# Kernel tuning notes

Measured on AMD Instinct MI355X. Metric: run time of the kernel, lower is better.

## Reference

```python
import jax, jax.numpy as jnp
import numpy as np

CONF_THRESH = 0.3
NMS_THRESH = 0.5
TOP_K = 64
VAR = (0.1, 0.2)  # standard SSD decode variances


def setup_inputs() -> dict:
    key = jax.random.key(0)
    k1, k2, k3 = jax.random.split(key, 3)
    B, A, C = 16, 16384, 81
    loc = jax.random.normal(k1, (B, A, 4), jnp.float32)
    conf = jax.random.normal(k2, (B, A, C), jnp.float32)
    anchors = jax.random.uniform(k3, (A, 4), jnp.float32)  # cxcywh in [0,1]
    return {"loc": loc, "conf": conf, "anchors": anchors}


def _decode(loc, anchors):
    # SSD-style decode: loc [A,4] offsets, anchors [A,4] cxcywh -> corners [A,4]
    cxcy = anchors[:, :2] + loc[:, :2] * VAR[0] * anchors[:, 2:]
    wh = anchors[:, 2:] * jnp.exp(loc[:, 2:] * VAR[1])
    tl = cxcy - wh * 0.5
    return jnp.concatenate([tl, tl + wh], axis=1)


def _iou(box, boxes):
    # box [4], boxes [A,4] in corner format
    tl = jnp.maximum(box[:2], boxes[:, :2])
    br = jnp.minimum(box[2:], boxes[:, 2:])
    wh = jnp.clip(br - tl, 0.0)
    inter = wh[:, 0] * wh[:, 1]
    a1 = (box[2] - box[0]) * (box[3] - box[1])
    a2 = (boxes[:, 2] - boxes[:, 0]) * (boxes[:, 3] - boxes[:, 1])
    return inter / (a1 + a2 - inter)


def _nms(boxes, scores):
    # greedy NMS for one (batch, class) lane; boxes [A,4], scores [A]
    s0 = jnp.where(scores > CONF_THRESH, scores, -1.0)

    def step(s, _):
        i = jnp.argmax(s)
        sc = s[i]
        box = boxes[i]
        keep = sc > 0.0  # -1 means masked/suppressed; valid scores > conf_thresh > 0
        supp = jnp.where(_iou(box, boxes) > NMS_THRESH, -1.0, s).at[i].set(-1.0)
        s_next = jnp.where(keep, supp, s)
        row = jnp.where(keep, jnp.concatenate([sc[None], box]),
                        jnp.zeros((5,), s.dtype))
        return s_next, row

    _, rows = jax.lax.scan(step, s0, None, length=TOP_K)
    return rows  # [TOP_K, 5] = (score, x1, y1, x2, y2), zero-padded


def reference(loc, conf, anchors):
    conf = jax.nn.sigmoid(conf)                      # [B,A,C]
    boxes = jax.vmap(_decode, in_axes=(0, None))(loc, anchors)  # [B,A,4]
    scores = jnp.swapaxes(conf, 1, 2)                # [B,C,A]
    per_class = jax.vmap(_nms, in_axes=(None, 0))    # over classes
    out = jax.vmap(per_class)(boxes, scores)         # [B,C,TOP_K,5]
    return out
```

## Files before the change

### kernel.cpp

```cpp
#include <hip/hip_runtime.h>
#include <math.h>

constexpr int B_N  = 16;
constexpr int A_N  = 16384;
constexpr int C_N  = 81;
constexpr int TOPK = 64;
constexpr int DNT  = 256;
constexpr int NBINS = 232;
constexpr int CAP   = 512;
constexpr unsigned BIN_BASE = 0x3E99u;

constexpr int TA   = 128;
constexpr int TPAD = 85;
constexpr int TNT  = 256;
constexpr int TILE_ELEMS = TA * C_N;
constexpr int TILE_F4    = (TA / 4) * C_N;

constexpr int HNT = 256;

__global__ __launch_bounds__(DNT) void decode_kernel(const float4* __restrict__ loc,
                                                     const float4* __restrict__ anch,
                                                     float4* __restrict__ boxes) {
    int i = blockIdx.x * DNT + threadIdx.x;
    int a = i & (A_N - 1);
    float4 l  = loc[i];
    float4 an = anch[a];
    float cx = an.x + (l.x * 0.1f) * an.z;
    float cy = an.y + (l.y * 0.1f) * an.w;
    float w  = an.z * expf(l.z * 0.2f);
    float h  = an.w * expf(l.w * 0.2f);
    float x1 = cx - w * 0.5f;
    float y1 = cy - h * 0.5f;
    boxes[i] = make_float4(x1, y1, x1 + w, y1 + h);
}

__global__ __launch_bounds__(TNT) void sigT_kernel(const float* __restrict__ conf,
                                                   float* __restrict__ scoresT) {
    __shared__ float tile[TA][TPAD];

    const int a0 = blockIdx.x * TA;
    const int b  = blockIdx.y;
    const int t  = threadIdx.x;

    const float* src = conf + ((size_t)b * A_N + a0) * C_N;
#pragma unroll
    for (int i = 0; i < (TILE_ELEMS + TNT - 1) / TNT; ++i) {
        int idx = i * TNT + t;
        if (idx < TILE_ELEMS) {
            float x  = src[idx];
            int   al = idx / C_N;
            int   cc = idx - al * C_N;
            tile[al][cc] = 1.0f / (1.0f + expf(-x));
        }
    }
    __syncthreads();
    float* dst = scoresT + (size_t)b * C_N * A_N + a0;
#pragma unroll
    for (int i = 0; i < (TILE_F4 + TNT - 1) / TNT; ++i) {
        int idx4 = i * TNT + t;
        if (idx4 < TILE_F4) {
            int cc  = idx4 >> 5;
            int al4 = idx4 & 31;
            float4 v;
            v.x = tile[al4 * 4 + 0][cc];
            v.y = tile[al4 * 4 + 1][cc];
            v.z = tile[al4 * 4 + 2][cc];
            v.w = tile[al4 * 4 + 3][cc];
            ((float4*)(dst + (size_t)cc * A_N))[al4] = v;
        }
    }
}

__global__ __launch_bounds__(HNT) void hist_kernel(const float* __restrict__ scoresT,
                                                   int* __restrict__ ghist) {
    __shared__ int hist[NBINS];
    const int bc = blockIdx.x;
    const int t  = threadIdx.x;
    for (int i = t; i < NBINS; i += HNT) hist[i] = 0;
    __syncthreads();
    const float4* sptr = (const float4*)(scoresT + (size_t)bc * A_N);
    for (int i = 0; i < A_N / 4 / HNT; ++i) {
        float4 s4 = sptr[t + HNT * i];
        float s[4] = {s4.x, s4.y, s4.z, s4.w};
#pragma unroll
        for (int q = 0; q < 4; ++q) {
            if (s[q] > 0.3f) {
                unsigned u = __float_as_uint(s[q]);
                int bin = (int)(u >> 16) - (int)BIN_BASE;
                bin = bin < 0 ? 0 : (bin > NBINS - 1 ? NBINS - 1 : bin);
                atomicAdd(&hist[bin], 1);
            }
        }
    }
    __syncthreads();
    int* g = ghist + (size_t)bc * NBINS;
    for (int i = t; i < NBINS; i += HNT) g[i] = hist[i];
}

template <bool TRANSPOSED>
__global__ __launch_bounds__(64, 4) void nms_kernel(const float* __restrict__ conf,
                                                    const float* __restrict__ scoresT,
                                                    const int* __restrict__ ghist,
                                                    const float4* __restrict__ boxes,
                                                    float* __restrict__ out) {
    __shared__ int hist[NBINS];
    __shared__ unsigned long long cand[CAP];
    __shared__ float4 cbox[CAP];
    __shared__ int s_cnt;

    const int c    = blockIdx.x;
    const int b    = blockIdx.y;
    const int lane = threadIdx.x;

    const float4* bptr = boxes + (size_t)b * A_N;
    const float4* sptr = (const float4*)(scoresT + ((size_t)b * C_N + c) * A_N);
    const float*  cptr = conf + (size_t)b * A_N * C_N + c;
    float* optr = out + ((size_t)(b * C_N + c)) * TOPK * 5;

    if (TRANSPOSED) {
        const int* g = ghist + (size_t)(b * C_N + c) * NBINS;
        for (int i = lane; i < NBINS; i += 64) hist[i] = g[i];
    } else {
        for (int i = lane; i < NBINS; i += 64) hist[i] = 0;
        __syncthreads();
        for (int i = 0; i < A_N / 256; ++i) {
            int a0 = 4 * (lane + 64 * i);
#pragma unroll
            for (int q = 0; q < 4; ++q) {
                float x = cptr[(size_t)(a0 + q) * C_N];
                float s = 1.0f / (1.0f + expf(-x));
                if (s > 0.3f) {
                    unsigned u = __float_as_uint(s);
                    int bin = (int)(u >> 16) - (int)BIN_BASE;
                    bin = bin < 0 ? 0 : (bin > NBINS - 1 ? NBINS - 1 : bin);
                    atomicAdd(&hist[bin], 1);
                }
            }
        }
    }
    __syncthreads();

    float rx1 = 0.f, ry1 = 0.f, rx2 = 0.f, ry2 = 0.f, rar = 0.f;
    int acc = 0, kout = 0;

    int bin_hi = NBINS;
    for (;;) {
        int lo = bin_hi, tot = 0;
        while (lo > 0) {
            int cnt = hist[lo - 1];
            if (tot + cnt > CAP) {
                if (tot == 0) { lo--; }
                break;
            }
            tot += cnt; lo--;
        }
        const int bin_lo = lo;
        if (bin_lo == bin_hi) break;
        if (lane == 0) s_cnt = 0;
        __syncthreads();

        for (int i = 0; i < A_N / 256; ++i) {
            float s[4];
            if (TRANSPOSED) {
                float4 s4 = sptr[lane + 64 * i];
                s[0] = s4.x; s[1] = s4.y; s[2] = s4.z; s[3] = s4.w;
            } else {
                int a0 = 4 * (lane + 64 * i);
#pragma unroll
                for (int q = 0; q < 4; ++q) {
                    float x = cptr[(size_t)(a0 + q) * C_N];
                    s[q] = 1.0f / (1.0f + expf(-x));
                }
            }
#pragma unroll
            for (int q = 0; q < 4; ++q) {
                if (s[q] > 0.3f) {
                    unsigned u = __float_as_uint(s[q]);
                    int bin = (int)(u >> 16) - (int)BIN_BASE;
                    bin = bin < 0 ? 0 : (bin > NBINS - 1 ? NBINS - 1 : bin);
                    if (bin >= bin_lo && bin < bin_hi) {
                        int slot = atomicAdd(&s_cnt, 1);
                        if (slot < CAP) {
                            unsigned a = (unsigned)(4 * (lane + 64 * i) + q);
                            cand[slot] = ((unsigned long long)u << 32) | (unsigned)(~a);
                        }
                    }
                }
            }
        }
        __syncthreads();
        int C = s_cnt; if (C > CAP) C = CAP;

        if (C > 0) {
            unsigned long long key[8];
#pragma unroll
            for (int r = 0; r < 8; ++r) {
                int sidx = r * 64 + lane;
                key[r] = (sidx < C) ? cand[sidx] : 0ull;
            }
#pragma unroll
            for (int k = 2; k <= CAP; k <<= 1) {
#pragma unroll
                for (int j = k >> 1; j > 0; j >>= 1) {
                    if (j >= 64) {
                        int jr = j >> 6;
#pragma unroll
                        for (int r = 0; r < 8; ++r) {
                            int rp = r ^ jr;
                            if (rp > r) {
                                int e = r * 64 + lane;
                                bool up = ((e & k) == 0);
                                unsigned long long va = key[r], vb = key[rp];
                                bool sw = up ? (va < vb) : (va > vb);
                                if (sw) { key[r] = vb; key[rp] = va; }
                            }
                        }
                    } else {
#pragma unroll
                        for (int r = 0; r < 8; ++r) {
                            int e = r * 64 + lane;
                            bool up    = ((e & k) == 0);
                            bool isLow = ((lane & j) == 0);
                            unsigned long long va = key[r];
                            unsigned long long vb = __shfl_xor(va, j, 64);
                            bool keepMax = (up == isLow);
                            key[r] = keepMax ? (va > vb ? va : vb)
                                             : (va < vb ? va : vb);
                        }
                    }
                }
            }
            __syncthreads();
#pragma unroll
            for (int r = 0; r < 8; ++r) cand[r * 64 + lane] = key[r];
            __syncthreads();

#pragma unroll
            for (int r = 0; r < 8; ++r) {
                int e = r * 64 + lane;
                if (e < C) {
                    int idx = (int)(~(unsigned)cand[e]);
                    cbox[e] = bptr[idx];
                }
            }
            __syncthreads();

            int t = 0;
            unsigned long long k0 = cand[0];
            float4 cb = cbox[0];
            while (t < C) {
                unsigned long long nk = 0ull;
                float4 nb = cb;
                if (t + 1 < C) { nk = cand[t + 1]; nb = cbox[t + 1]; }
                float sc = __uint_as_float((unsigned)(k0 >> 32));
                float ca = (cb.z - cb.x) * (cb.w - cb.y);
                bool over = false;
                if (lane < acc) {
                    float tlx = fmaxf(rx1, cb.x);
                    float tly = fmaxf(ry1, cb.y);
                    float brx = fminf(rx2, cb.z);
                    float bry = fminf(ry2, cb.w);
                    float iw  = fmaxf(brx - tlx, 0.0f);
                    float ih  = fmaxf(bry - tly, 0.0f);
                    float inter = iw * ih;
                    float iou = inter / (rar + ca - inter);
                    over = iou > 0.5f;
                }
                if (!__any(over)) {
                    if (lane == acc) { rx1 = cb.x; ry1 = cb.y; rx2 = cb.z; ry2 = cb.w; rar = ca; }
                    if (lane == 0) {
                        float* o = optr + (size_t)kout * 5;
                        o[0] = sc; o[1] = cb.x; o[2] = cb.y; o[3] = cb.z; o[4] = cb.w;
                    }
                    acc++; kout++;
                    if (acc == TOPK) break;
                }
                ++t; k0 = nk; cb = nb;
            }
        }
        if (acc == TOPK) break;
        bin_hi = bin_lo;
    }

    {
        float* o  = optr + (size_t)kout * 5;
        int   rem = (TOPK - kout) * 5;
        for (int t = lane; t < rem; t += 64) o[t] = 0.0f;
    }
}

extern "C" void kernel_launch(void* const* d_in, const int* in_sizes, int n_in,
                              void* d_out, int out_size, void* d_ws, size_t ws_size,
                              hipStream_t stream) {
    const float* loc     = (const float*)d_in[0];
    const float* conf    = (const float*)d_in[1];
    const float* anchors = (const float*)d_in[2];
    float* out = (float*)d_out;

    const size_t boxes_bytes  = (size_t)B_N * A_N * sizeof(float4);
    const size_t scores_bytes = (size_t)B_N * C_N * A_N * sizeof(float);
    const size_t hist_bytes   = (size_t)B_N * C_N * NBINS * sizeof(int);

    float4* boxes = (float4*)d_ws;

    decode_kernel<<<(B_N * A_N) / DNT, DNT, 0, stream>>>(
        (const float4*)loc, (const float4*)anchors, boxes);

    if (ws_size >= boxes_bytes + scores_bytes + hist_bytes) {
        float* scoresT = (float*)((char*)d_ws + boxes_bytes);
        int*   ghist   = (int*)((char*)d_ws + boxes_bytes + scores_bytes);
        sigT_kernel<<<dim3(A_N / TA, B_N), TNT, 0, stream>>>(conf, scoresT);
        hist_kernel<<<dim3(B_N * C_N), HNT, 0, stream>>>(scoresT, ghist);
        nms_kernel<true><<<dim3(C_N, B_N), 64, 0, stream>>>(conf, scoresT, ghist, boxes, out);
    } else {
        nms_kernel<false><<<dim3(C_N, B_N), 64, 0, stream>>>(conf, nullptr, nullptr, boxes, out);
    }
}
```

Baseline: 254.3 us.

## Move first-round candidate selection into wide histogram kernel

```diff
diff --git a/kernel.cpp b/kernel.cpp
--- a/kernel.cpp
+++ b/kernel.cpp
@@ -16,7 +16,7 @@
 constexpr int TILE_ELEMS = TA * C_N;
 constexpr int TILE_F4    = (TA / 4) * C_N;
 
-constexpr int HNT = 256;
+constexpr int SNT = 256;
 
 __global__ __launch_bounds__(DNT) void decode_kernel(const float4* __restrict__ loc,
                                                      const float4* __restrict__ anch,
@@ -71,16 +71,20 @@
     }
 }
 
-__global__ __launch_bounds__(HNT) void hist_kernel(const float* __restrict__ scoresT,
-                                                   int* __restrict__ ghist) {
+__global__ __launch_bounds__(SNT) void select_kernel(const float* __restrict__ scoresT,
+                                                     int* __restrict__ ghist,
+                                                     unsigned long long* __restrict__ gcand,
+                                                     int2* __restrict__ gmeta) {
     __shared__ int hist[NBINS];
+    __shared__ int s_cnt;
     const int bc = blockIdx.x;
     const int t  = threadIdx.x;
-    for (int i = t; i < NBINS; i += HNT) hist[i] = 0;
-    __syncthreads();
+    for (int i = t; i < NBINS; i += SNT) hist[i] = 0;
+    __syncthreads();
+
     const float4* sptr = (const float4*)(scoresT + (size_t)bc * A_N);
-    for (int i = 0; i < A_N / 4 / HNT; ++i) {
-        float4 s4 = sptr[t + HNT * i];
+    for (int i = 0; i < A_N / 4 / SNT; ++i) {
+        float4 s4 = sptr[t + SNT * i];
         float s[4] = {s4.x, s4.y, s4.z, s4.w};
 #pragma unroll
         for (int q = 0; q < 4; ++q) {
@@ -94,13 +98,141 @@
     }
     __syncthreads();
     int* g = ghist + (size_t)bc * NBINS;
-    for (int i = t; i < NBINS; i += HNT) g[i] = hist[i];
-}
-
-template <bool TRANSPOSED>
+    for (int i = t; i < NBINS; i += SNT) g[i] = hist[i];
+
+    int lo = NBINS, tot = 0;
+    while (lo > 0) {
+        int cnt = hist[lo - 1];
+        if (tot + cnt > CAP) {
+            if (tot == 0) { lo--; }
+            break;
+        }
+        tot += cnt; lo--;
+    }
+    if (t == 0) s_cnt = 0;
+    __syncthreads();
+
+    unsigned long long* cd = gcand + (size_t)bc * CAP;
+    for (int i = 0; i < A_N / 4 / SNT; ++i) {
+        float4 s4 = sptr[t + SNT * i];
+        float s[4] = {s4.x, s4.y, s4.z, s4.w};
+#pragma unroll
+        for (int q = 0; q < 4; ++q) {
+            if (s[q] > 0.3f) {
+                unsigned u = __float_as_uint(s[q]);
+                int bin = (int)(u >> 16) - (int)BIN_BASE;
+                bin = bin < 0 ? 0 : (bin > NBINS - 1 ? NBINS - 1 : bin);
+                if (bin >= lo) {
+                    int slot = atomicAdd(&s_cnt, 1);
+                    if (slot < CAP) {
+                        unsigned a = (unsigned)(4 * (t + SNT * i) + q);
+                        cd[slot] = ((unsigned long long)u << 32) | (unsigned)(~a);
+                    }
+                }
+            }
+        }
+    }
+    __syncthreads();
+    if (t == 0) {
+        int C = s_cnt; if (C > CAP) C = CAP;
+        gmeta[bc] = make_int2(C, lo);
+    }
+}
+
+__device__ __forceinline__ void sort_gather_scan(
+        unsigned long long* cand, float4* cbox, int C, int lane,
+        const float4* __restrict__ bptr, float* __restrict__ optr,
+        float& rx1, float& ry1, float& rx2, float& ry2, float& rar,
+        int& acc, int& kout) {
+    unsigned long long key[8];
+#pragma unroll
+    for (int r = 0; r < 8; ++r) {
+        int sidx = r * 64 + lane;
+        key[r] = (sidx < C) ? cand[sidx] : 0ull;
+    }
+#pragma unroll
+    for (int k = 2; k <= CAP; k <<= 1) {
+#pragma unroll
+        for (int j = k >> 1; j > 0; j >>= 1) {
+            if (j >= 64) {
+                int jr = j >> 6;
+#pragma unroll
+                for (int r = 0; r < 8; ++r) {
+                    int rp = r ^ jr;
+                    if (rp > r) {
+                        int e = r * 64 + lane;
+                        bool up = ((e & k) == 0);
+                        unsigned long long va = key[r], vb = key[rp];
+                        bool sw = up ? (va < vb) : (va > vb);
+                        if (sw) { key[r] = vb; key[rp] = va; }
+                    }
+                }
+            } else {
+#pragma unroll
+                for (int r = 0; r < 8; ++r) {
+                    int e = r * 64 + lane;
+                    bool up    = ((e & k) == 0);
+                    bool isLow = ((lane & j) == 0);
+                    unsigned long long va = key[r];
+                    unsigned long long vb = __shfl_xor(va, j, 64);
+                    bool keepMax = (up == isLow);
+                    key[r] = keepMax ? (va > vb ? va : vb)
+                                     : (va < vb ? va : vb);
+                }
+            }
+        }
+    }
+    __syncthreads();
+#pragma unroll
+    for (int r = 0; r < 8; ++r) cand[r * 64 + lane] = key[r];
+    __syncthreads();
+#pragma unroll
+    for (int r = 0; r < 8; ++r) {
+        int e = r * 64 + lane;
+        if (e < C) cbox[e] = bptr[(int)(~(unsigned)cand[e])];
+    }
+    __syncthreads();
+
+    int t = 0;
+    unsigned long long k0 = cand[0];
+    float4 cb = cbox[0];
+    while (t < C) {
+        unsigned long long nk = 0ull;
+        float4 nb = cb;
+        if (t + 1 < C) { nk = cand[t + 1]; nb = cbox[t + 1]; }
+        float sc = __uint_as_float((unsigned)(k0 >> 32));
+        float ca = (cb.z - cb.x) * (cb.w - cb.y);
+        bool over = false;
+        if (lane < acc) {
+            float tlx = fmaxf(rx1, cb.x);
+            float tly = fmaxf(ry1, cb.y);
+            float brx = fminf(rx2, cb.z);
+            float bry = fminf(ry2, cb.w);
+            float iw  = fmaxf(brx - tlx, 0.0f);
+            float ih  = fmaxf(bry - tly, 0.0f);
+            float inter = iw * ih;
+            float iou = inter / (rar + ca - inter);
+            over = iou > 0.5f;
+        }
+        if (!__any(over)) {
+            if (lane == acc) { rx1 = cb.x; ry1 = cb.y; rx2 = cb.z; ry2 = cb.w; rar = ca; }
+            if (lane == 0) {
+                float* o = optr + (size_t)kout * 5;
+                o[0] = sc; o[1] = cb.x; o[2] = cb.y; o[3] = cb.z; o[4] = cb.w;
+            }
+            acc++; kout++;
+            if (acc == TOPK) break;
+        }
+        ++t; k0 = nk; cb = nb;
+    }
+}
+
+template <bool PRESEL>
 __global__ __launch_bounds__(64, 4) void nms_kernel(const float* __restrict__ conf,
                                                     const float* __restrict__ scoresT,
                                                     const int* __restrict__ ghist,
+                                                    const unsigned long long* __restrict__ gcand,
+                                                    const int2* __restrict__ gmeta,
                                                     const float4* __restrict__ boxes,
                                                     float* __restrict__ out) {
     __shared__ int hist[NBINS];
@@ -110,16 +242,36 @@
 
     const int c    = blockIdx.x;
     const int b    = blockIdx.y;
+    const int bc   = b * C_N + c;
     const int lane = threadIdx.x;
 
     const float4* bptr = boxes + (size_t)b * A_N;
-    const float4* sptr = (const float4*)(scoresT + ((size_t)b * C_N + c) * A_N);
+    const float4* sptr = (const float4*)(scoresT + (size_t)bc * A_N);
     const float*  cptr = conf + (size_t)b * A_N * C_N + c;
-    float* optr = out + ((size_t)(b * C_N + c)) * TOPK * 5;
-
-    if (TRANSPOSED) {
-        const int* g = ghist + (size_t)(b * C_N + c) * NBINS;
-        for (int i = lane; i < NBINS; i += 64) hist[i] = g[i];
+    float* optr = out + (size_t)bc * TOPK * 5;
+
+    float rx1 = 0.f, ry1 = 0.f, rx2 = 0.f, ry2 = 0.f, rar = 0.f;
+    int acc = 0, kout = 0;
+    int bin_hi;
+
+    if (PRESEL) {
+        int2 meta = gmeta[bc];
+        int C = meta.x;
+        bin_hi = meta.y;
+        const unsigned long long* cd = gcand + (size_t)bc * CAP;
+#pragma unroll
+        for (int r = 0; r < 8; ++r) {
+            int e = r * 64 + lane;
+            cand[e] = (e < C) ? cd[e] : 0ull;
+        }
+        __syncthreads();
+        if (C > 0)
+            sort_gather_scan(cand, cbox, C, lane, bptr, optr,
+                             rx1, ry1, rx2, ry2, rar, acc, kout);
+        if (acc < TOPK && bin_hi > 0) {
+            for (int i = lane; i < NBINS; i += 64) hist[i] = ghist[(size_t)bc * NBINS + i];
+            __syncthreads();
+        }
     } else {
         for (int i = lane; i < NBINS; i += 64) hist[i] = 0;
         __syncthreads();
@@ -137,14 +289,11 @@
                 }
             }
         }
-    }
-    __syncthreads();
-
-    float rx1 = 0.f, ry1 = 0.f, rx2 = 0.f, ry2 = 0.f, rar = 0.f;
-    int acc = 0, kout = 0;
-
-    int bin_hi = NBINS;
-    for (;;) {
+        __syncthreads();
+        bin_hi = NBINS;
+    }
+
+    while (acc < TOPK) {
         int lo = bin_hi, tot = 0;
         while (lo > 0) {
             int cnt = hist[lo - 1];
@@ -161,7 +310,7 @@
 
         for (int i = 0; i < A_N / 256; ++i) {
             float s[4];
-            if (TRANSPOSED) {
+            if (PRESEL) {
                 float4 s4 = sptr[lane + 64 * i];
                 s[0] = s4.x; s[1] = s4.y; s[2] = s4.z; s[3] = s4.w;
             } else {
@@ -190,95 +339,9 @@
         }
         __syncthreads();
         int C = s_cnt; if (C > CAP) C = CAP;
-
-        if (C > 0) {
-            unsigned long long key[8];
-#pragma unroll
-            for (int r = 0; r < 8; ++r) {
-                int sidx = r * 64 + lane;
-                key[r] = (sidx < C) ? cand[sidx] : 0ull;
-            }
-#pragma unroll
-            for (int k = 2; k <= CAP; k <<= 1) {
-#pragma unroll
-                for (int j = k >> 1; j > 0; j >>= 1) {
-                    if (j >= 64) {
-                        int jr = j >> 6;
-#pragma unroll
-                        for (int r = 0; r < 8; ++r) {
-                            int rp = r ^ jr;
-                            if (rp > r) {
-                                int e = r * 64 + lane;
-                                bool up = ((e & k) == 0);
-                                unsigned long long va = key[r], vb = key[rp];
-                                bool sw = up ? (va < vb) : (va > vb);
-                                if (sw) { key[r] = vb; key[rp] = va; }
-                            }
-                        }
-                    } else {
-#pragma unroll
-                        for (int r = 0; r < 8; ++r) {
-                            int e = r * 64 + lane;
-                            bool up    = ((e & k) == 0);
-                            bool isLow = ((lane & j) == 0);
-                            unsigned long long va = key[r];
-                            unsigned long long vb = __shfl_xor(va, j, 64);
-                            bool keepMax = (up == isLow);
-                            key[r] = keepMax ? (va > vb ? va : vb)
-                                             : (va < vb ? va : vb);
-                        }
-                    }
-                }
-            }
-            __syncthreads();
-#pragma unroll
-            for (int r = 0; r < 8; ++r) cand[r * 64 + lane] = key[r];
-            __syncthreads();
-
-#pragma unroll
-            for (int r = 0; r < 8; ++r) {
-                int e = r * 64 + lane;
-                if (e < C) {
-                    int idx = (int)(~(unsigned)cand[e]);
-                    cbox[e] = bptr[idx];
-                }
-            }
-            __syncthreads();
-
-            int t = 0;
-            unsigned long long k0 = cand[0];
-            float4 cb = cbox[0];
-            while (t < C) {
-                unsigned long long nk = 0ull;
-                float4 nb = cb;
-                if (t + 1 < C) { nk = cand[t + 1]; nb = cbox[t + 1]; }
-                float sc = __uint_as_float((unsigned)(k0 >> 32));
-                float ca = (cb.z - cb.x) * (cb.w - cb.y);
-                bool over = false;
-                if (lane < acc) {
-                    float tlx = fmaxf(rx1, cb.x);
-                    float tly = fmaxf(ry1, cb.y);
-                    float brx = fminf(rx2, cb.z);
-                    float bry = fminf(ry2, cb.w);
-                    float iw  = fmaxf(brx - tlx, 0.0f);
-                    float ih  = fmaxf(bry - tly, 0.0f);
-                    float inter = iw * ih;
-                    float iou = inter / (rar + ca - inter);
-                    over = iou > 0.5f;
-                }
-                if (!__any(over)) {
-                    if (lane == acc) { rx1 = cb.x; ry1 = cb.y; rx2 = cb.z; ry2 = cb.w; rar = ca; }
-                    if (lane == 0) {
-                        float* o = optr + (size_t)kout * 5;
-                        o[0] = sc; o[1] = cb.x; o[2] = cb.y; o[3] = cb.z; o[4] = cb.w;
-                    }
-                    acc++; kout++;
-                    if (acc == TOPK) break;
-                }
-                ++t; k0 = nk; cb = nb;
-            }
-        }
-        if (acc == TOPK) break;
+        if (C > 0)
+            sort_gather_scan(cand, cbox, C, lane, bptr, optr,
+                             rx1, ry1, rx2, ry2, rar, acc, kout);
         bin_hi = bin_lo;
     }
 
@@ -300,19 +363,24 @@
     const size_t boxes_bytes  = (size_t)B_N * A_N * sizeof(float4);
     const size_t scores_bytes = (size_t)B_N * C_N * A_N * sizeof(float);
     const size_t hist_bytes   = (size_t)B_N * C_N * NBINS * sizeof(int);
+    const size_t cand_bytes   = (size_t)B_N * C_N * CAP * sizeof(unsigned long long);
+    const size_t meta_bytes   = (size_t)B_N * C_N * sizeof(int2);
 
     float4* boxes = (float4*)d_ws;
 
     decode_kernel<<<(B_N * A_N) / DNT, DNT, 0, stream>>>(
         (const float4*)loc, (const float4*)anchors, boxes);
 
-    if (ws_size >= boxes_bytes + scores_bytes + hist_bytes) {
-        float* scoresT = (float*)((char*)d_ws + boxes_bytes);
-        int*   ghist   = (int*)((char*)d_ws + boxes_bytes + scores_bytes);
+    if (ws_size >= boxes_bytes + scores_bytes + hist_bytes + cand_bytes + meta_bytes) {
+        char* p = (char*)d_ws + boxes_bytes;
+        float* scoresT            = (float*)p;              p += scores_bytes;
+        int*   ghist              = (int*)p;                p += hist_bytes;
+        unsigned long long* gcand = (unsigned long long*)p; p += cand_bytes;
+        int2*  gmeta              = (int2*)p;
         sigT_kernel<<<dim3(A_N / TA, B_N), TNT, 0, stream>>>(conf, scoresT);
-        hist_kernel<<<dim3(B_N * C_N), HNT, 0, stream>>>(scoresT, ghist);
-        nms_kernel<true><<<dim3(C_N, B_N), 64, 0, stream>>>(conf, scoresT, ghist, boxes, out);
+        select_kernel<<<dim3(B_N * C_N), SNT, 0, stream>>>(scoresT, ghist, gcand, gmeta);
+        nms_kernel<true><<<dim3(C_N, B_N), 64, 0, stream>>>(conf, scoresT, ghist, gcand, gmeta, boxes, out);
     } else {
-        nms_kernel<false><<<dim3(C_N, B_N), 64, 0, stream>>>(conf, nullptr, nullptr, boxes, out);
-    }
-}
+        nms_kernel<false><<<dim3(C_N, B_N), 64, 0, stream>>>(conf, nullptr, nullptr, nullptr, nullptr, boxes, out);
+    }
+}
```

Result: faster. 224.7 us (-11.7%).
